# Kernel optimization log

Hardware: AMD Instinct MI355X
Metric: run time of the kernel (lower is better)

## Reference

```python
import jax, jax.numpy as jnp
import numpy as np

N_NODES = 100000
N_REL = 8
IN_DIM = 64
HID = 128
OUT = 64
N_EDGES = 640000


def setup_inputs() -> dict:
    key = jax.random.key(0)
    ks = jax.random.split(key, 24)

    def w(k, shape, fan_in):
        return jax.random.normal(k, shape, jnp.float32) / np.sqrt(fan_in).astype(np.float32)

    inp = {}
    inp["emb"] = jax.random.normal(ks[0], (N_NODES, IN_DIM), jnp.float32)
    dims = [(IN_DIM, HID), (HID, HID), (HID, HID // 2), (HID // 2, OUT)]
    for i, (di, do) in enumerate(dims, 1):
        inp[f"W{i}"] = w(ks[3 * i], (N_REL, di, do), di)      # per-relation weight
        inp[f"R{i}"] = w(ks[3 * i + 1], (di, do), di)          # root weight
        inp[f"B{i}"] = jnp.zeros((do,), jnp.float32)           # bias
    inp["g1"] = jnp.ones((HID,), jnp.float32)
    inp["b1"] = jnp.zeros((HID,), jnp.float32)
    inp["g2"] = jnp.ones((HID,), jnp.float32)
    inp["b2"] = jnp.zeros((HID,), jnp.float32)
    inp["ei"] = jax.random.randint(ks[20], (2, N_EDGES), 0, N_NODES, jnp.int32)
    inp["et"] = jax.random.randint(ks[21], (N_EDGES,), 0, N_REL, jnp.int32)
    return inp


def rgcn(x, ei, et, W, Wr, b):
    # PyG RGCNConv (aggr='mean'): out_i = x_i @ Wroot + b + sum_r mean_{j in N_r(i)} x_j @ W_r
    # Aggregate-then-transform: mean x[src] per (dst, rel) bin, then per-relation GEMM.
    n, r, d = x.shape[0], W.shape[0], x.shape[1]
    src, dst = ei[0], ei[1]
    seg = dst * r + et                                   # combined (node, relation) segment id
    agg = jax.ops.segment_sum(x[src], seg, num_segments=n * r)          # [N*R, d]
    cnt = jax.ops.segment_sum(jnp.ones((src.shape[0],), x.dtype), seg, num_segments=n * r)
    agg = (agg / jnp.maximum(cnt, 1.0)[:, None]).reshape(n, r, d)       # mean per relation
    return jnp.einsum('nri,rio->no', agg, W) + x @ Wr + b


def layer_norm(x, g, b, eps=1e-5):
    mu = jnp.mean(x, axis=-1, keepdims=True)
    var = jnp.mean((x - mu) ** 2, axis=-1, keepdims=True)
    return (x - mu) * jax.lax.rsqrt(var + eps) * g + b


def reference(emb, W1, R1, B1, W2, R2, B2, W3, R3, B3, W4, R4, B4, g1, b1, g2, b2, ei, et):
    # dropout is eval-mode identity
    x = jax.nn.relu(rgcn(emb, ei, et, W1, R1, B1))
    x = layer_norm(x, g1, b1)
    identity = x
    x = jax.nn.relu(rgcn(x, ei, et, W2, R2, B2))
    x = layer_norm(x + identity, g2, b2)
    x = jax.nn.relu(rgcn(x, ei, et, W3, R3, B3))
    return rgcn(x, ei, et, W4, R4, B4)
```

## Files before the change

kernel.cpp:

```cpp
#include <hip/hip_runtime.h>
#include <math.h>

#define NN 100000
#define NR 8
#define NE 640000
#define SEGN (NN * NR)
#define SPB 2048
#define NSB ((SEGN + SPB - 1) / SPB)

#define TILES 1563
#define HT1 782
#define HT2 781
#define HP1 (HT1 * 64)
#define HP2 (HT2 * 64)
#define HPF (TILES * 64)

typedef __attribute__((ext_vector_type(8))) __bf16 bf16x8;
typedef __attribute__((ext_vector_type(4))) float  f32x4;

__device__ __forceinline__ float bf2f(unsigned short b) {
    return __uint_as_float((unsigned)b << 16);
}
__device__ __forceinline__ unsigned short f2bf(float v) {
    __bf16 b = (__bf16)v;
    return __builtin_bit_cast(unsigned short, b);
}


__global__ __launch_bounds__(256) void count_kernel(
    const int* __restrict__ dst, const int* __restrict__ et, unsigned* __restrict__ cnt) {
    int e = blockIdx.x * 256 + threadIdx.x;
    if (e < NE) atomicAdd(&cnt[(size_t)et[e] * NN + dst[e]], 1u);
}

__global__ __launch_bounds__(256) void scan1_kernel(
    const unsigned* __restrict__ cnt, unsigned* __restrict__ bsum) {
    __shared__ unsigned red[256];
    int b = blockIdx.x, t = threadIdx.x;
    int i0 = b * SPB;
    unsigned s = 0;
#pragma unroll
    for (int k = 0; k < SPB / 256; ++k) {
        int i = i0 + k * 256 + t;
        if (i < SEGN) s += cnt[i];
    }
    red[t] = s;
    __syncthreads();
    for (int off = 128; off >= 1; off >>= 1) {
        if (t < off) red[t] += red[t + off];
        __syncthreads();
    }
    if (t == 0) bsum[b] = red[0];
}

__global__ __launch_bounds__(512) void scan2_kernel(
    unsigned* __restrict__ bsum, int* __restrict__ segoff) {
    __shared__ unsigned buf[512];
    int t = threadIdx.x;
    unsigned v = (t < NSB) ? bsum[t] : 0u;
    buf[t] = v;
    __syncthreads();
    for (int off = 1; off < 512; off <<= 1) {
        unsigned w = (t >= off) ? buf[t - off] : 0u;
        __syncthreads();
        buf[t] += w;
        __syncthreads();
    }
    if (t < NSB) bsum[t] = buf[t] - v;
    if (t == 0) segoff[SEGN] = NE;
}

__global__ __launch_bounds__(256) void scan3_kernel(
    const unsigned* __restrict__ cnt, const unsigned* __restrict__ bsum,
    int* __restrict__ segoff) {
    __shared__ unsigned lc[SPB];
    __shared__ unsigned tsum[256];
    int b = blockIdx.x, t = threadIdx.x;
    int i0 = b * SPB;
#pragma unroll
    for (int k = 0; k < SPB / 256; ++k) {
        int i = i0 + k * 256 + t;
        lc[k * 256 + t] = (i < SEGN) ? cnt[i] : 0u;
    }
    __syncthreads();
    unsigned s = 0;
#pragma unroll
    for (int k = 0; k < 8; ++k) s += lc[t * 8 + k];
    tsum[t] = s;
    __syncthreads();
    for (int off = 1; off < 256; off <<= 1) {
        unsigned w = (t >= off) ? tsum[t - off] : 0u;
        __syncthreads();
        tsum[t] += w;
        __syncthreads();
    }
    unsigned base = bsum[b] + tsum[t] - s;
#pragma unroll
    for (int k = 0; k < 8; ++k) {
        unsigned c = lc[t * 8 + k];
        lc[t * 8 + k] = base;
        base += c;
    }
    __syncthreads();
#pragma unroll
    for (int k = 0; k < SPB / 256; ++k) {
        int i = i0 + k * 256 + t;
        if (i < SEGN) segoff[i] = (int)lc[k * 256 + t];
    }
}

__global__ __launch_bounds__(256) void fill_kernel(
    const int* __restrict__ src, const int* __restrict__ dst, const int* __restrict__ et,
    const int* __restrict__ segoff, unsigned* __restrict__ cursor, int* __restrict__ esrc) {
    int e = blockIdx.x * 256 + threadIdx.x;
    if (e >= NE) return;
    int d = dst[e];
    int seg = et[e] * NN + d;
    int pos = segoff[seg] + (int)atomicAdd(&cursor[seg], 1u);
    esrc[pos] = src[e] | ((d & 3) << 17);
}


template <int D, int O>
__global__ __launch_bounds__(256) void pack_kernel(
    const float* __restrict__ W, const float* __restrict__ Wr, __bf16* __restrict__ Wp) {
    constexpr int KT = D / 32, NTN = O / 16;
    int idx = blockIdx.x * 256 + threadIdx.x;
    if (idx >= (NR + 1) * KT * NTN * 64) return;
    int l = idx & 63;
    int rest = idx >> 6;
    int nt = rest % NTN; rest /= NTN;
    int kt = rest % KT;
    int r  = rest / KT;
    const float* srcw = (r < NR) ? (W + (size_t)r * D * O) : Wr;
    int n  = nt * 16 + (l & 15);
    int k0 = kt * 32 + (l >> 4) * 8;
    bf16x8 v;
#pragma unroll
    for (int j = 0; j < 8; ++j) {
        int p  = k0 + j;
        int kd = (D == 128) ? ((p >> 1) + ((p & 1) << 6)) : p;
        v[j] = (__bf16)srcw[(size_t)kd * O + n];
    }
    *(bf16x8*)(Wp + (size_t)idx * 8) = v;
}


template <int D, int XF>
__global__ __launch_bounds__(256) void gather_kernel(
    const void* __restrict__ xin, const int* __restrict__ segoff,
    const int* __restrict__ esrc, ushort* __restrict__ agg,
    int base, int HP)
{
    int wv = threadIdx.x >> 6, ln = threadIdx.x & 63;
    int r  = blockIdx.y;
    int i0 = blockIdx.x * 16 + wv * 4;
    int n0 = base + i0;

    const float*    xf = (const float*)xin;
    const ushort*   xb = (const ushort*)xin;
    const unsigned* xs = (const unsigned*)xin;

    if (r < 8) {
        float ax[4] = {0, 0, 0, 0}, ay[4] = {0, 0, 0, 0};
        int eo[5];
#pragma unroll
        for (int k = 0; k <= 4; ++k) {
            int node = n0 + k; if (node > NN) node = NN;
            eo[k] = segoff[r * NN + node];
        }
        for (int ei = eo[0]; ei < eo[4]; ei += 4) {
            int nb = eo[4] - ei; if (nb > 4) nb = 4;
            int mm[4]; float vx[4], vy[4];
#pragma unroll
            for (int b = 0; b < 4; ++b) mm[b] = (b < nb) ? esrc[ei + b] : 0;
#pragma unroll
            for (int b = 0; b < 4; ++b) {
                if (b < nb) {
                    int s = mm[b] & 0x1FFFF;
                    if constexpr (XF == 0) {
                        vx[b] = xf[(size_t)s * 64 + ln];
                    } else if constexpr (XF == 1) {
                        unsigned w = xs[(size_t)s * 64 + ln];
                        vx[b] = bf2f((unsigned short)(w & 0xFFFFu));
                        vy[b] = bf2f((unsigned short)(w >> 16));
                    } else {
                        vx[b] = bf2f(xb[(size_t)s * 64 + ln]);
                    }
                }
            }
#pragma unroll
            for (int b = 0; b < 4; ++b) {
                if (b < nb) {
                    int k = mm[b] >> 17;
#pragma unroll
                    for (int kk = 0; kk < 4; ++kk) {
                        ax[kk] += (kk == k) ? vx[b] : 0.0f;
                        if constexpr (D == 128) ay[kk] += (kk == k) ? vy[b] : 0.0f;
                    }
                }
            }
        }
#pragma unroll
        for (int k = 0; k < 4; ++k) {
            int c = eo[k + 1] - eo[k];
            float sc = (c > 0) ? 1.0f / (float)c : 0.0f;
            size_t row = ((size_t)r * HP + i0 + k) * D;
            if constexpr (D == 128) {
                unsigned st = (unsigned)f2bf(ax[k] * sc) | ((unsigned)f2bf(ay[k] * sc) << 16);
                __builtin_nontemporal_store(st, (unsigned*)(agg + row) + ln);
            } else {
                __builtin_nontemporal_store(f2bf(ax[k] * sc), agg + row + ln);
            }
        }
    } else {
#pragma unroll
        for (int k = 0; k < 4; ++k) {
            int n = n0 + k;
            size_t row = ((size_t)8 * HP + i0 + k) * D;
            if constexpr (D == 128) {
                unsigned w = 0;
                if (n < NN) w = xs[(size_t)n * 64 + ln];
                __builtin_nontemporal_store(w, (unsigned*)(agg + row) + ln);
            } else {
                ushort w = 0;
                if (n < NN) {
                    if constexpr (XF == 0) w = f2bf(xf[(size_t)n * 64 + ln]);
                    else                   w = xb[(size_t)n * 64 + ln];
                }
                __builtin_nontemporal_store(w, agg + row + ln);
            }
        }
    }
}


template <int D, int O, int MODE, int OF>
__global__ __launch_bounds__(256) void gemm_layer(
    const ushort* __restrict__ agg, const __bf16* __restrict__ Wp,
    const float* __restrict__ bias, const float* __restrict__ gamma,
    const float* __restrict__ beta, const unsigned* __restrict__ xres,
    void* __restrict__ outv, int base, int HP)
{
    constexpr int KT = D / 32, NTN = O / 16;
    int t = threadIdx.x, wv = t >> 6, ln = t & 63, lg = ln >> 4, lm = ln & 15;
    int i0 = blockIdx.x * 64;

    f32x4 acc[NTN];
#pragma unroll
    for (int nt = 0; nt < NTN; ++nt)
#pragma unroll
        for (int q = 0; q < 4; ++q) acc[nt][q] = 0.0f;

    const ushort* abase = agg + ((size_t)(i0 + wv * 16 + lm)) * D + lg * 8;

#pragma unroll 1
    for (int r = 0; r < 9; ++r) {
        const ushort* ar = abase + (size_t)r * HP * D;
        const __bf16* bp = Wp + (((size_t)(r * KT) * NTN) << 9) + (ln << 3);
#pragma unroll
        for (int kt = 0; kt < KT; ++kt) {
            bf16x8 A = __builtin_nontemporal_load((const bf16x8*)(ar + kt * 32));
            const __bf16* bpk = bp + (((size_t)(kt * NTN)) << 9);
#pragma unroll
            for (int nt = 0; nt < NTN; ++nt) {
                bf16x8 B = *(const bf16x8*)(bpk + ((size_t)nt << 9));
                acc[nt] = __builtin_amdgcn_mfma_f32_16x16x32_bf16(A, B, acc[nt], 0, 0, 0);
            }
        }
    }

    float bb[NTN], gg[NTN], be[NTN];
#pragma unroll
    for (int nt = 0; nt < NTN; ++nt) {
        bb[nt] = bias[nt * 16 + lm];
        if constexpr (MODE <= 1) {
            gg[nt] = gamma[nt * 16 + lm];
            be[nt] = beta[nt * 16 + lm];
        } else {
            gg[nt] = 0.0f; be[nt] = 0.0f;
        }
    }
#pragma unroll
    for (int q = 0; q < 4; ++q) {
        int row = wv * 16 + lg * 4 + q;
        int n = base + i0 + row;
        int nc = (n < NN) ? n : 0;
        float v[NTN];
#pragma unroll
        for (int nt = 0; nt < NTN; ++nt) {
            v[nt] = acc[nt][q] + bb[nt];
            if constexpr (MODE <= 2) v[nt] = fmaxf(v[nt], 0.0f);
            if constexpr (MODE == 1) {
                unsigned w = xres[(size_t)nc * 64 + (nt & 3) * 16 + lm];
                v[nt] += bf2f((unsigned short)((nt < 4) ? (w & 0xFFFFu) : (w >> 16)));
            }
        }
        if constexpr (MODE <= 1) {
            float s1 = 0.0f, s2 = 0.0f;
#pragma unroll
            for (int nt = 0; nt < NTN; ++nt) { s1 += v[nt]; s2 += v[nt] * v[nt]; }
#pragma unroll
            for (int off = 1; off < 16; off <<= 1) {
                s1 += __shfl_xor(s1, off, 64);
                s2 += __shfl_xor(s2, off, 64);
            }
            float mu  = s1 * (1.0f / O);
            float var = s2 * (1.0f / O) - mu * mu;
            float rs  = rsqrtf(var + 1e-5f);
#pragma unroll
            for (int nt = 0; nt < NTN; ++nt) v[nt] = (v[nt] - mu) * rs * gg[nt] + be[nt];
        }
        if (n < NN) {
            if constexpr (OF == 0) {
#pragma unroll
                for (int nt = 0; nt < NTN; ++nt)
                    __builtin_nontemporal_store(
                        v[nt], (float*)outv + (size_t)n * O + nt * 16 + lm);
            } else if constexpr (OF == 1) {
#pragma unroll
                for (int nt = 0; nt < 4; ++nt)
                    ((unsigned*)outv)[(size_t)n * 64 + nt * 16 + lm] =
                        (unsigned)f2bf(v[nt]) | ((unsigned)f2bf(v[nt + 4]) << 16);
            } else {
#pragma unroll
                for (int nt = 0; nt < NTN; ++nt)
                    ((ushort*)outv)[(size_t)n * 64 + nt * 16 + lm] = f2bf(v[nt]);
            }
        }
    }
}


extern "C" void kernel_launch(void* const* d_in, const int* in_sizes, int n_in,
                              void* d_out, int out_size, void* d_ws, size_t ws_size,
                              hipStream_t stream) {
    const float* emb = (const float*)d_in[0];
    const float* W1  = (const float*)d_in[1];
    const float* R1  = (const float*)d_in[2];
    const float* B1  = (const float*)d_in[3];
    const float* W2  = (const float*)d_in[4];
    const float* R2  = (const float*)d_in[5];
    const float* B2  = (const float*)d_in[6];
    const float* W3  = (const float*)d_in[7];
    const float* R3  = (const float*)d_in[8];
    const float* B3  = (const float*)d_in[9];
    const float* W4  = (const float*)d_in[10];
    const float* R4  = (const float*)d_in[11];
    const float* B4  = (const float*)d_in[12];
    const float* g1  = (const float*)d_in[13];
    const float* b1  = (const float*)d_in[14];
    const float* g2  = (const float*)d_in[15];
    const float* b2  = (const float*)d_in[16];
    const int*   ei  = (const int*)d_in[17];
    const int*   et  = (const int*)d_in[18];
    const int* srcp = ei;
    const int* dstp = ei + NE;

    char* ws = (char*)d_ws;
    if (ws_size < 185734160u) return;
    int*      segoff = (int*)(ws + 0);
    int*      esrc   = (int*)(ws + 3200016);
    __bf16*   Wp1    = (__bf16*)(ws + 5760016);
    __bf16*   Wp2    = (__bf16*)(ws + 5907472);
    __bf16*   Wp3    = (__bf16*)(ws + 6202384);
    __bf16*   Wp4    = (__bf16*)(ws + 6349840);
    void*     x1     = (void*)(ws + 6423568);
    void*     x2     = (void*)(ws + 32023568);
    void*     x3     = (void*)(ws + 57623568);
    ushort*   agg    = (ushort*)(ws + 70423568);
    unsigned* cnt    = (unsigned*)(ws + 70423568);
    unsigned* cursor = (unsigned*)(ws + 73623568);
    unsigned* bsum   = (unsigned*)(ws + 76823568);
    float*    outp   = (float*)d_out;

    hipMemsetAsync(cnt, 0, 3200000, stream);
    hipMemsetAsync(cursor, 0, 3200000, stream);

    count_kernel<<<(NE + 255) / 256, 256, 0, stream>>>(dstp, et, cnt);
    scan1_kernel<<<NSB, 256, 0, stream>>>(cnt, bsum);
    scan2_kernel<<<1, 512, 0, stream>>>(bsum, segoff);
    scan3_kernel<<<NSB, 256, 0, stream>>>(cnt, bsum, segoff);
    fill_kernel<<<(NE + 255) / 256, 256, 0, stream>>>(
        srcp, dstp, et, segoff, cursor, esrc);

    pack_kernel<64, 128><<<(9 * 2 * 8 * 64 + 255) / 256, 256, 0, stream>>>(W1, R1, Wp1);
    pack_kernel<128, 128><<<(9 * 4 * 8 * 64 + 255) / 256, 256, 0, stream>>>(W2, R2, Wp2);
    pack_kernel<128, 64><<<(9 * 4 * 4 * 64 + 255) / 256, 256, 0, stream>>>(W3, R3, Wp3);
    pack_kernel<64, 64><<<(9 * 2 * 4 * 64 + 255) / 256, 256, 0, stream>>>(W4, R4, Wp4);

    gather_kernel<64, 0><<<dim3(HPF / 16, 9), 256, 0, stream>>>(emb, segoff, esrc, agg, 0, HPF);
    gemm_layer<64, 128, 0, 1><<<TILES, 256, 0, stream>>>(
        agg, Wp1, B1, g1, b1, nullptr, x1, 0, HPF);

    gather_kernel<128, 1><<<dim3(HP1 / 16, 9), 256, 0, stream>>>(x1, segoff, esrc, agg, 0, HP1);
    gemm_layer<128, 128, 1, 1><<<HT1, 256, 0, stream>>>(
        agg, Wp2, B2, g2, b2, (const unsigned*)x1, x2, 0, HP1);
    gather_kernel<128, 1><<<dim3(HP2 / 16, 9), 256, 0, stream>>>(x1, segoff, esrc, agg, HP1, HP2);
    gemm_layer<128, 128, 1, 1><<<HT2, 256, 0, stream>>>(
        agg, Wp2, B2, g2, b2, (const unsigned*)x1, x2, HP1, HP2);

    gather_kernel<128, 1><<<dim3(HP1 / 16, 9), 256, 0, stream>>>(x2, segoff, esrc, agg, 0, HP1);
    gemm_layer<128, 64, 2, 2><<<HT1, 256, 0, stream>>>(
        agg, Wp3, B3, nullptr, nullptr, nullptr, x3, 0, HP1);
    gather_kernel<128, 1><<<dim3(HP2 / 16, 9), 256, 0, stream>>>(x2, segoff, esrc, agg, HP1, HP2);
    gemm_layer<128, 64, 2, 2><<<HT2, 256, 0, stream>>>(
        agg, Wp3, B3, nullptr, nullptr, nullptr, x3, HP1, HP2);

    gather_kernel<64, 2><<<dim3(HPF / 16, 9), 256, 0, stream>>>(x3, segoff, esrc, agg, 0, HPF);
    gemm_layer<64, 64, 3, 0><<<TILES, 256, 0, stream>>>(
        agg, Wp4, B4, nullptr, nullptr, nullptr, outp, 0, HPF);
}
```

Measured before the change: 864.7 us.

## Read root features directly in GEMM and split gathers for cache locality

Drops the ninth 'root' slice of the aggregation buffer: the GEMM now loads the node's own features straight from the input activation (fp32 converted on the fly, or bf16), so the gather no longer copies x into agg. Each gather is also split into two half-range launches, and nontemporal stores and loads are replaced by normal ones, so agg slices may stay in L2/MALL for the following GEMM. This saves one write and one read of a full feature copy per layer, at the cost of extra kernel launches and fp32-to-bf16 conversion inside the GEMM for layer 1.

```diff
diff --git a/kernel.cpp b/kernel.cpp
--- a/kernel.cpp
+++ b/kernel.cpp
@@ -150,97 +150,77 @@
 __global__ __launch_bounds__(256) void gather_kernel(
     const void* __restrict__ xin, const int* __restrict__ segoff,
     const int* __restrict__ esrc, ushort* __restrict__ agg,
-    int base, int HP)
+    int nbase, int agg_off, int HP)
 {
     int wv = threadIdx.x >> 6, ln = threadIdx.x & 63;
     int r  = blockIdx.y;
     int i0 = blockIdx.x * 16 + wv * 4;
-    int n0 = base + i0;
+    int n0 = nbase + i0;
 
     const float*    xf = (const float*)xin;
     const ushort*   xb = (const ushort*)xin;
     const unsigned* xs = (const unsigned*)xin;
 
-    if (r < 8) {
-        float ax[4] = {0, 0, 0, 0}, ay[4] = {0, 0, 0, 0};
-        int eo[5];
-#pragma unroll
-        for (int k = 0; k <= 4; ++k) {
-            int node = n0 + k; if (node > NN) node = NN;
-            eo[k] = segoff[r * NN + node];
-        }
-        for (int ei = eo[0]; ei < eo[4]; ei += 4) {
-            int nb = eo[4] - ei; if (nb > 4) nb = 4;
-            int mm[4]; float vx[4], vy[4];
-#pragma unroll
-            for (int b = 0; b < 4; ++b) mm[b] = (b < nb) ? esrc[ei + b] : 0;
-#pragma unroll
-            for (int b = 0; b < 4; ++b) {
-                if (b < nb) {
-                    int s = mm[b] & 0x1FFFF;
-                    if constexpr (XF == 0) {
-                        vx[b] = xf[(size_t)s * 64 + ln];
-                    } else if constexpr (XF == 1) {
-                        unsigned w = xs[(size_t)s * 64 + ln];
-                        vx[b] = bf2f((unsigned short)(w & 0xFFFFu));
-                        vy[b] = bf2f((unsigned short)(w >> 16));
-                    } else {
-                        vx[b] = bf2f(xb[(size_t)s * 64 + ln]);
-                    }
+    float ax[4] = {0, 0, 0, 0}, ay[4] = {0, 0, 0, 0};
+    int eo[5];
+#pragma unroll
+    for (int k = 0; k <= 4; ++k) {
+        int node = n0 + k; if (node > NN) node = NN;
+        eo[k] = segoff[r * NN + node];
+    }
+    for (int ei = eo[0]; ei < eo[4]; ei += 4) {
+        int nb = eo[4] - ei; if (nb > 4) nb = 4;
+        int mm[4]; float vx[4], vy[4];
+#pragma unroll
+        for (int b = 0; b < 4; ++b) mm[b] = (b < nb) ? esrc[ei + b] : 0;
+#pragma unroll
+        for (int b = 0; b < 4; ++b) {
+            if (b < nb) {
+                int s = mm[b] & 0x1FFFF;
+                if constexpr (XF == 0) {
+                    vx[b] = xf[(size_t)s * 64 + ln];
+                } else if constexpr (XF == 1) {
+                    unsigned w = xs[(size_t)s * 64 + ln];
+                    vx[b] = bf2f((unsigned short)(w & 0xFFFFu));
+                    vy[b] = bf2f((unsigned short)(w >> 16));
+                } else {
+                    vx[b] = bf2f(xb[(size_t)s * 64 + ln]);
                 }
             }
-#pragma unroll
-            for (int b = 0; b < 4; ++b) {
-                if (b < nb) {
-                    int k = mm[b] >> 17;
-#pragma unroll
-                    for (int kk = 0; kk < 4; ++kk) {
-                        ax[kk] += (kk == k) ? vx[b] : 0.0f;
-                        if constexpr (D == 128) ay[kk] += (kk == k) ? vy[b] : 0.0f;
-                    }
+        }
+#pragma unroll
+        for (int b = 0; b < 4; ++b) {
+            if (b < nb) {
+                int k = mm[b] >> 17;
+#pragma unroll
+                for (int kk = 0; kk < 4; ++kk) {
+                    ax[kk] += (kk == k) ? vx[b] : 0.0f;
+                    if constexpr (D == 128) ay[kk] += (kk == k) ? vy[b] : 0.0f;
                 }
             }
         }
-#pragma unroll
-        for (int k = 0; k < 4; ++k) {
-            int c = eo[k + 1] - eo[k];
-            float sc = (c > 0) ? 1.0f / (float)c : 0.0f;
-            size_t row = ((size_t)r * HP + i0 + k) * D;
-            if constexpr (D == 128) {
-                unsigned st = (unsigned)f2bf(ax[k] * sc) | ((unsigned)f2bf(ay[k] * sc) << 16);
-                __builtin_nontemporal_store(st, (unsigned*)(agg + row) + ln);
-            } else {
-                __builtin_nontemporal_store(f2bf(ax[k] * sc), agg + row + ln);
-            }
-        }
-    } else {
-#pragma unroll
-        for (int k = 0; k < 4; ++k) {
-            int n = n0 + k;
-            size_t row = ((size_t)8 * HP + i0 + k) * D;
-            if constexpr (D == 128) {
-                unsigned w = 0;
-                if (n < NN) w = xs[(size_t)n * 64 + ln];
-                __builtin_nontemporal_store(w, (unsigned*)(agg + row) + ln);
-            } else {
-                ushort w = 0;
-                if (n < NN) {
-                    if constexpr (XF == 0) w = f2bf(xf[(size_t)n * 64 + ln]);
-                    else                   w = xb[(size_t)n * 64 + ln];
-                }
-                __builtin_nontemporal_store(w, agg + row + ln);
-            }
-        }
-    }
-}
-
-
-template <int D, int O, int MODE, int OF>
+    }
+#pragma unroll
+    for (int k = 0; k < 4; ++k) {
+        int c = eo[k + 1] - eo[k];
+        float sc = (c > 0) ? 1.0f / (float)c : 0.0f;
+        size_t row = ((size_t)r * HP + agg_off + i0 + k) * D;
+        if constexpr (D == 128) {
+            unsigned st = (unsigned)f2bf(ax[k] * sc) | ((unsigned)f2bf(ay[k] * sc) << 16);
+            *((unsigned*)(agg + row) + ln) = st;
+        } else {
+            agg[row + ln] = f2bf(ax[k] * sc);
+        }
+    }
+}
+
+
+template <int D, int O, int MODE, int XF, int OF>
 __global__ __launch_bounds__(256) void gemm_layer(
     const ushort* __restrict__ agg, const __bf16* __restrict__ Wp,
     const float* __restrict__ bias, const float* __restrict__ gamma,
     const float* __restrict__ beta, const unsigned* __restrict__ xres,
-    void* __restrict__ outv, int base, int HP)
+    const void* __restrict__ xroot, void* __restrict__ outv, int base, int HP)
 {
     constexpr int KT = D / 32, NTN = O / 16;
     int t = threadIdx.x, wv = t >> 6, ln = t & 63, lg = ln >> 4, lm = ln & 15;
@@ -255,12 +235,38 @@
     const ushort* abase = agg + ((size_t)(i0 + wv * 16 + lm)) * D + lg * 8;
 
 #pragma unroll 1
-    for (int r = 0; r < 9; ++r) {
+    for (int r = 0; r < 8; ++r) {
         const ushort* ar = abase + (size_t)r * HP * D;
         const __bf16* bp = Wp + (((size_t)(r * KT) * NTN) << 9) + (ln << 3);
 #pragma unroll
         for (int kt = 0; kt < KT; ++kt) {
-            bf16x8 A = __builtin_nontemporal_load((const bf16x8*)(ar + kt * 32));
+            bf16x8 A = *(const bf16x8*)(ar + kt * 32);
+            const __bf16* bpk = bp + (((size_t)(kt * NTN)) << 9);
+#pragma unroll
+            for (int nt = 0; nt < NTN; ++nt) {
+                bf16x8 B = *(const bf16x8*)(bpk + ((size_t)nt << 9));
+                acc[nt] = __builtin_amdgcn_mfma_f32_16x16x32_bf16(A, B, acc[nt], 0, 0, 0);
+            }
+        }
+    }
+    {
+        int nrow = base + i0 + wv * 16 + lm;
+        if (nrow >= NN) nrow = NN - 1;
+        const __bf16* bp = Wp + (((size_t)(8 * KT) * NTN) << 9) + (ln << 3);
+#pragma unroll
+        for (int kt = 0; kt < KT; ++kt) {
+            bf16x8 A;
+            if constexpr (XF == 0) {
+                const float* xp = (const float*)xroot + (size_t)nrow * 64 + kt * 32 + lg * 8;
+                f32x4 a0 = *(const f32x4*)xp;
+                f32x4 a1 = *(const f32x4*)(xp + 4);
+#pragma unroll
+                for (int j = 0; j < 4; ++j) { A[j] = (__bf16)a0[j]; A[j + 4] = (__bf16)a1[j]; }
+            } else if constexpr (XF == 1) {
+                A = *(const bf16x8*)((const ushort*)xroot + (size_t)nrow * 128 + kt * 32 + lg * 8);
+            } else {
+                A = *(const bf16x8*)((const ushort*)xroot + (size_t)nrow * 64 + kt * 32 + lg * 8);
+            }
             const __bf16* bpk = bp + (((size_t)(kt * NTN)) << 9);
 #pragma unroll
             for (int nt = 0; nt < NTN; ++nt) {
@@ -389,25 +395,31 @@
     pack_kernel<128, 64><<<(9 * 4 * 4 * 64 + 255) / 256, 256, 0, stream>>>(W3, R3, Wp3);
     pack_kernel<64, 64><<<(9 * 2 * 4 * 64 + 255) / 256, 256, 0, stream>>>(W4, R4, Wp4);
 
-    gather_kernel<64, 0><<<dim3(HPF / 16, 9), 256, 0, stream>>>(emb, segoff, esrc, agg, 0, HPF);
-    gemm_layer<64, 128, 0, 1><<<TILES, 256, 0, stream>>>(
-        agg, Wp1, B1, g1, b1, nullptr, x1, 0, HPF);
-
-    gather_kernel<128, 1><<<dim3(HP1 / 16, 9), 256, 0, stream>>>(x1, segoff, esrc, agg, 0, HP1);
-    gemm_layer<128, 128, 1, 1><<<HT1, 256, 0, stream>>>(
-        agg, Wp2, B2, g2, b2, (const unsigned*)x1, x2, 0, HP1);
-    gather_kernel<128, 1><<<dim3(HP2 / 16, 9), 256, 0, stream>>>(x1, segoff, esrc, agg, HP1, HP2);
-    gemm_layer<128, 128, 1, 1><<<HT2, 256, 0, stream>>>(
-        agg, Wp2, B2, g2, b2, (const unsigned*)x1, x2, HP1, HP2);
-
-    gather_kernel<128, 1><<<dim3(HP1 / 16, 9), 256, 0, stream>>>(x2, segoff, esrc, agg, 0, HP1);
-    gemm_layer<128, 64, 2, 2><<<HT1, 256, 0, stream>>>(
-        agg, Wp3, B3, nullptr, nullptr, nullptr, x3, 0, HP1);
-    gather_kernel<128, 1><<<dim3(HP2 / 16, 9), 256, 0, stream>>>(x2, segoff, esrc, agg, HP1, HP2);
-    gemm_layer<128, 64, 2, 2><<<HT2, 256, 0, stream>>>(
-        agg, Wp3, B3, nullptr, nullptr, nullptr, x3, HP1, HP2);
-
-    gather_kernel<64, 2><<<dim3(HPF / 16, 9), 256, 0, stream>>>(x3, segoff, esrc, agg, 0, HPF);
-    gemm_layer<64, 64, 3, 0><<<TILES, 256, 0, stream>>>(
-        agg, Wp4, B4, nullptr, nullptr, nullptr, outp, 0, HPF);
-}
+    gather_kernel<64, 0><<<dim3(HP1 / 16, 8), 256, 0, stream>>>(emb, segoff, esrc, agg, 0, 0, HPF);
+    gather_kernel<64, 0><<<dim3(HP2 / 16, 8), 256, 0, stream>>>(emb, segoff, esrc, agg, HP1, HP1, HPF);
+    gemm_layer<64, 128, 0, 0, 1><<<TILES, 256, 0, stream>>>(
+        agg, Wp1, B1, g1, b1, nullptr, emb, x1, 0, HPF);
+
+    gather_kernel<128, 1><<<dim3(25024 / 16, 8), 256, 0, stream>>>(x1, segoff, esrc, agg, 0, 0, HP1);
+    gather_kernel<128, 1><<<dim3(25024 / 16, 8), 256, 0, stream>>>(x1, segoff, esrc, agg, 25024, 25024, HP1);
+    gemm_layer<128, 128, 1, 1, 1><<<HT1, 256, 0, stream>>>(
+        agg, Wp2, B2, g2, b2, (const unsigned*)x1, x1, x2, 0, HP1);
+    gather_kernel<128, 1><<<dim3(25024 / 16, 8), 256, 0, stream>>>(x1, segoff, esrc, agg, HP1, 0, HP2);
+    gather_kernel<128, 1><<<dim3(24960 / 16, 8), 256, 0, stream>>>(x1, segoff, esrc, agg, HP1 + 25024, 25024, HP2);
+    gemm_layer<128, 128, 1, 1, 1><<<HT2, 256, 0, stream>>>(
+        agg, Wp2, B2, g2, b2, (const unsigned*)x1, x1, x2, HP1, HP2);
+
+    gather_kernel<128, 1><<<dim3(25024 / 16, 8), 256, 0, stream>>>(x2, segoff, esrc, agg, 0, 0, HP1);
+    gather_kernel<128, 1><<<dim3(25024 / 16, 8), 256, 0, stream>>>(x2, segoff, esrc, agg, 25024, 25024, HP1);
+    gemm_layer<128, 64, 2, 1, 2><<<HT1, 256, 0, stream>>>(
+        agg, Wp3, B3, nullptr, nullptr, nullptr, x2, x3, 0, HP1);
+    gather_kernel<128, 1><<<dim3(25024 / 16, 8), 256, 0, stream>>>(x2, segoff, esrc, agg, HP1, 0, HP2);
+    gather_kernel<128, 1><<<dim3(24960 / 16, 8), 256, 0, stream>>>(x2, segoff, esrc, agg, HP1 + 25024, 25024, HP2);
+    gemm_layer<128, 64, 2, 1, 2><<<HT2, 256, 0, stream>>>(
+        agg, Wp3, B3, nullptr, nullptr, nullptr, x2, x3, HP1, HP2);
+
+    gather_kernel<64, 2><<<dim3(HP1 / 16, 8), 256, 0, stream>>>(x3, segoff, esrc, agg, 0, 0, HPF);
+    gather_kernel<64, 2><<<dim3(HP2 / 16, 8), 256, 0, stream>>>(x3, segoff, esrc, agg, HP1, HP1, HPF);
+    gemm_layer<64, 64, 3, 2, 0><<<TILES, 256, 0, stream>>>(
+        agg, Wp4, B4, nullptr, nullptr, nullptr, x3, outp, 0, HPF);
+}
```

Result: faster. 782.5 us (-9.5%).
